# Performance work log

Hardware: AMD Instinct MI355X
Metric: run time of the kernel (lower is better)

The kernel has to match this reference:

```python
import jax, jax.numpy as jnp
from jax import lax
import numpy as np

N = 65536
D = 512
NUM_STEPS = 10
TIME_INTERVAL = 1.0


def setup_inputs() -> dict:
    key = jax.random.key(0)
    ks = jax.random.split(key, 8)
    s1 = 1.0 / np.sqrt(D + 1)
    s2 = 1.0 / np.sqrt(D)
    sg = 1.0 / np.sqrt(2 * D)
    return {
        "current_node_features": jax.random.normal(ks[0], (N, D), jnp.float32),
        "previous_hidden_state": jax.random.normal(ks[1], (N, D), jnp.float32),
        # torch nn.Linear layout: weight [out, in], bias [out]
        "W1": jax.random.uniform(ks[2], (D, D + 1), jnp.float32, -s1, s1),
        "b1": jax.random.uniform(ks[3], (D,), jnp.float32, -s1, s1),
        "W2": jax.random.uniform(ks[4], (D, D), jnp.float32, -s2, s2),
        "b2": jax.random.uniform(ks[5], (D,), jnp.float32, -s2, s2),
        "Wg": jax.random.uniform(ks[6], (D, 2 * D), jnp.float32, -sg, sg),
        "bg": jax.random.uniform(ks[7], (D,), jnp.float32, -sg, sg),
    }


def reference(current_node_features, previous_hidden_state, W1, b1, W2, b2, Wg, bg):
    x = current_node_features
    dt = jnp.asarray(TIME_INTERVAL / NUM_STEPS, x.dtype)
    n = x.shape[0]

    def euler_step(h, t):
        # concat time feature: [N, D+1]
        time_col = jnp.full((n, 1), t, h.dtype)
        z = jnp.concatenate([h, time_col], axis=-1)
        deriv = jnp.tanh(jnp.tanh(z @ W1.T + b1) @ W2.T + b2)
        return h + dt * deriv, None

    ts = jnp.arange(NUM_STEPS, dtype=x.dtype) * dt  # t_i = start + i*dt
    evolved, _ = lax.scan(euler_step, previous_hidden_state, ts)

    combined = jnp.concatenate([x, evolved], axis=-1)  # [N, 2D]
    gate = jax.nn.sigmoid(combined @ Wg.T + bg)
    updated = gate * evolved + (1.0 - gate) * x
    return updated, updated
```

## Files before the change

kernel.cpp:

```cpp
#include <hip/hip_runtime.h>

#define N_ROWS 65536
#define DIM    512
#define NSTEP  10

typedef float  f32x16 __attribute__((ext_vector_type(16)));
typedef float  f32x4  __attribute__((ext_vector_type(4)));
typedef short  s16x8  __attribute__((ext_vector_type(8)));
typedef __bf16 bf16x8 __attribute__((ext_vector_type(8)));
typedef unsigned int u32x2 __attribute__((ext_vector_type(2)));
typedef unsigned int u32x4 __attribute__((ext_vector_type(4)));

__device__ __forceinline__ unsigned f2bf(float f) {
  unsigned u = __float_as_uint(f);
  return (u + 0x7fffu + ((u >> 16) & 1u)) >> 16;
}
__device__ __forceinline__ unsigned pack2bf_rn(float a, float b) {
  unsigned ua = __float_as_uint(a) + 0x8000u;
  unsigned ub = __float_as_uint(b) + 0x8000u;
  return __builtin_amdgcn_perm(ub, ua, 0x07060302u);
}
#define LOG2E_X2 2.885390081777927f
#define LOG2E    1.442695040888963f
__device__ __forceinline__ float ftanh(float x) {
  float t = __builtin_amdgcn_exp2f(x * LOG2E_X2);
  float r = __builtin_amdgcn_rcpf(1.0f + t);
  return __builtin_fmaf(-2.0f, r, 1.0f);
}
__device__ __forceinline__ float fsigm(float x) {
  float t = __builtin_amdgcn_exp2f(-x * LOG2E);
  return __builtin_amdgcn_rcpf(1.0f + t);
}
__device__ __forceinline__ void mfma(f32x16& c, s16x8 a, s16x8 b) {
  c = __builtin_amdgcn_mfma_f32_32x32x16_bf16(
        __builtin_bit_cast(bf16x8, a), __builtin_bit_cast(bf16x8, b), c, 0, 0, 0);
}

__global__ void pack_frags_kernel(const float* __restrict__ src, int row_stride,
                                  int col_off, unsigned short* __restrict__ dst) {
  const int idx = blockIdx.x * 256 + threadIdx.x;
  const int l    = idx & 63;
  const int frag = idx >> 6;
  const int ks   = frag >> 4;
  const int otg  = frag & 15;
  const int o = otg * 32 + (l & 31);
  const int k = ks * 16 + (l >> 5) * 8;
  const float* p = src + (size_t)o * row_stride + col_off + k;
  s16x8 v;
#pragma unroll
  for (int i = 0; i < 8; ++i) v[i] = (short)f2bf(p[i]);
  *reinterpret_cast<s16x8*>(dst + (size_t)idx * 8) = v;
}

__global__ void c1_kernel(const float* __restrict__ W1, const float* __restrict__ b1,
                          float* __restrict__ c1) {
  const int o = threadIdx.x;
  const float wt = W1[(size_t)o * 513 + 512];
  const float bb = b1[o];
  for (int s = 0; s < NSTEP; ++s)
    c1[s * DIM + o] = bb + ((float)s * 0.1f) * wt;
}

__global__ __launch_bounds__(1024)
void ode_fused(const float* __restrict__ x, const float* __restrict__ h0,
               const float* __restrict__ b2, const float* __restrict__ bg,
               const unsigned short* __restrict__ w1f, const unsigned short* __restrict__ w2f,
               const unsigned short* __restrict__ wgaf, const unsigned short* __restrict__ wgbf,
               const float* __restrict__ c1, float* __restrict__ out)
{
  __shared__ char ldsT[64 * 1024];

  const int tid = threadIdx.x;
  const int w   = tid >> 6;
  const int l   = tid & 63;
  const int lm  = l & 31;
  const int h5  = l >> 5;
  const int m0  = blockIdx.x << 6;
  const int ow  = w << 5;
  const int rot = blockIdx.x & 31;

  {
    const int r  = tid >> 4;
    const int c0 = (tid & 15) << 2;
    const float* src = h0 + (size_t)(m0 + r) * DIM;
    char* trow = ldsT + r * 1024;
    const unsigned sw = (r & 7) << 4;
#pragma unroll
    for (int j = 0; j < 8; ++j) {
      const int c = c0 + (j << 6);
      f32x4 v = *reinterpret_cast<const f32x4*>(src + c);
      u32x2 pk;
      pk[0] = pack2bf_rn(v[0], v[1]);
      pk[1] = pack2bf_rn(v[2], v[3]);
      *reinterpret_cast<u32x2*>(trow + (((unsigned)(c << 1)) ^ sw)) = pk;
    }
  }

  f32x16 hst[2];
#pragma unroll
  for (int mt = 0; mt < 2; ++mt) {
    const float* hr = h0 + (size_t)(m0 + (mt << 5) + lm) * DIM;
#pragma unroll
    for (int g = 0; g < 4; ++g) {
      const int oc = ow + (g << 3) + (h5 << 2);
      f32x4 v = *reinterpret_cast<const f32x4*>(hr + oc);
#pragma unroll
      for (int j = 0; j < 4; ++j) hst[mt][(g << 2) + j] = v[j];
    }
  }

  const unsigned bm0 = (unsigned)lm << 10;
  const unsigned bm1 = (unsigned)(lm + 32) << 10;
  const unsigned sxm = (lm & 7) << 4;
  const unsigned kh  = (unsigned)h5 << 4;

  f32x16 acc[2];

  auto mm_lds = [&](const unsigned short* __restrict__ AF, const char* buf) {
    const s16x8* A = reinterpret_cast<const s16x8*>(AF);
#pragma unroll 4
    for (int ks = 0; ks < 32; ++ks) {
      const int kk = (ks + rot) & 31;
      s16x8 a = A[(((kk << 4) + w) << 6) + l];
      const unsigned ko = (((unsigned)kk << 5) + kh) ^ sxm;
      s16x8 b0 = *reinterpret_cast<const s16x8*>(buf + (bm0 + ko));
      s16x8 b1 = *reinterpret_cast<const s16x8*>(buf + (bm1 + ko));
      mfma(acc[0], a, b0);
      mfma(acc[1], a, b1);
    }
  };

  auto acc_init = [&](const float* __restrict__ vec) {
#pragma unroll
    for (int g = 0; g < 4; ++g) {
      const int oc = ow + (g << 3) + (h5 << 2);
      f32x4 v = *reinterpret_cast<const f32x4*>(vec + oc);
#pragma unroll
      for (int j = 0; j < 4; ++j) {
        acc[0][(g << 2) + j] = v[j];
        acc[1][(g << 2) + j] = v[j];
      }
    }
  };

  auto tile_write = [&](const f32x16 src[2], char* buf) {
#pragma unroll
    for (int mt = 0; mt < 2; ++mt) {
      const unsigned m = (unsigned)((mt << 5) + lm);
      char* trow = buf + (m << 10);
      const unsigned sw = (m & 7) << 4;
#pragma unroll
      for (int g = 0; g < 4; ++g) {
        const unsigned oc = (unsigned)(ow + (g << 3) + (h5 << 2));
        u32x2 pk;
        pk[0] = pack2bf_rn(src[mt][(g << 2) + 0], src[mt][(g << 2) + 1]);
        pk[1] = pack2bf_rn(src[mt][(g << 2) + 2], src[mt][(g << 2) + 3]);
        *reinterpret_cast<u32x2*>(trow + ((oc << 1) ^ sw)) = pk;
      }
    }
  };

  __syncthreads();

  for (int s = 0; s < NSTEP; ++s) {
    acc_init(c1 + s * DIM);
    mm_lds(w1f, ldsT);
#pragma unroll
    for (int mt = 0; mt < 2; ++mt)
#pragma unroll
      for (int i = 0; i < 16; ++i) acc[mt][i] = ftanh(acc[mt][i]);
    __syncthreads();
    tile_write(acc, ldsT);
    __syncthreads();
    acc_init(b2);
    mm_lds(w2f, ldsT);
#pragma unroll
    for (int mt = 0; mt < 2; ++mt)
#pragma unroll
      for (int i = 0; i < 16; ++i) {
        float t = __builtin_amdgcn_exp2f(acc[mt][i] * LOG2E_X2);
        float r = __builtin_amdgcn_rcpf(1.0f + t);
        hst[mt][i] = __builtin_fmaf(-0.2f, r, hst[mt][i] + 0.1f);
      }
    __syncthreads();
    tile_write(hst, ldsT);
    __syncthreads();
  }

  acc_init(bg);
  mm_lds(wgbf, ldsT);
  {
    const s16x8* A = reinterpret_cast<const s16x8*>(wgaf);
    const float* xr0 = x + (size_t)(m0 + lm) * DIM;
    const float* xr1 = x + (size_t)(m0 + 32 + lm) * DIM;
#pragma unroll 2
    for (int ks = 0; ks < 32; ++ks) {
      const int kk = (ks + rot) & 31;
      s16x8 a = A[(((kk << 4) + w) << 6) + l];
      const int kc = (kk << 4) + (h5 << 3);
      f32x4 u0 = *reinterpret_cast<const f32x4*>(xr0 + kc);
      f32x4 u1 = *reinterpret_cast<const f32x4*>(xr0 + kc + 4);
      u32x4 pb;
      pb[0] = pack2bf_rn(u0[0], u0[1]); pb[1] = pack2bf_rn(u0[2], u0[3]);
      pb[2] = pack2bf_rn(u1[0], u1[1]); pb[3] = pack2bf_rn(u1[2], u1[3]);
      s16x8 b0 = __builtin_bit_cast(s16x8, pb);
      f32x4 w0 = *reinterpret_cast<const f32x4*>(xr1 + kc);
      f32x4 w1 = *reinterpret_cast<const f32x4*>(xr1 + kc + 4);
      u32x4 qb;
      qb[0] = pack2bf_rn(w0[0], w0[1]); qb[1] = pack2bf_rn(w0[2], w0[3]);
      qb[2] = pack2bf_rn(w1[0], w1[1]); qb[3] = pack2bf_rn(w1[2], w1[3]);
      s16x8 b1 = __builtin_bit_cast(s16x8, qb);
      mfma(acc[0], a, b0);
      mfma(acc[1], a, b1);
    }
  }

  float* out1 = out + (size_t)N_ROWS * DIM;
#pragma unroll
  for (int mt = 0; mt < 2; ++mt) {
    const int m = m0 + (mt << 5) + lm;
    const float* xr = x + (size_t)m * DIM;
    float* o0p = out  + (size_t)m * DIM;
    float* o1p = out1 + (size_t)m * DIM;
#pragma unroll
    for (int g = 0; g < 4; ++g) {
      const int oc = ow + (g << 3) + (h5 << 2);
      f32x4 xv = *reinterpret_cast<const f32x4*>(xr + oc);
      f32x4 r;
#pragma unroll
      for (int j = 0; j < 4; ++j) {
        const float gt = fsigm(acc[mt][(g << 2) + j]);
        const float ev = hst[mt][(g << 2) + j];
        r[j] = gt * ev + (1.0f - gt) * xv[j];
      }
      *reinterpret_cast<f32x4*>(o0p + oc) = r;
      *reinterpret_cast<f32x4*>(o1p + oc) = r;
    }
  }
}

extern "C" void kernel_launch(void* const* d_in, const int* in_sizes, int n_in,
                              void* d_out, int out_size, void* d_ws, size_t ws_size,
                              hipStream_t stream) {
  const float* x  = (const float*)d_in[0];
  const float* h0 = (const float*)d_in[1];
  const float* W1 = (const float*)d_in[2];
  const float* b1 = (const float*)d_in[3];
  const float* W2 = (const float*)d_in[4];
  const float* b2 = (const float*)d_in[5];
  const float* Wg = (const float*)d_in[6];
  const float* bg = (const float*)d_in[7];

  char* ws = (char*)d_ws;
  const size_t FRAG_BYTES = (size_t)512 * 512 * 2;
  unsigned short* w1f  = (unsigned short*)(ws + 0 * FRAG_BYTES);
  unsigned short* w2f  = (unsigned short*)(ws + 1 * FRAG_BYTES);
  unsigned short* wgaf = (unsigned short*)(ws + 2 * FRAG_BYTES);
  unsigned short* wgbf = (unsigned short*)(ws + 3 * FRAG_BYTES);
  float*          c1   = (float*)(ws + 4 * FRAG_BYTES);

  pack_frags_kernel<<<128, 256, 0, stream>>>(W1, 513, 0,   w1f);
  pack_frags_kernel<<<128, 256, 0, stream>>>(W2, 512, 0,   w2f);
  pack_frags_kernel<<<128, 256, 0, stream>>>(Wg, 1024, 0,  wgaf);
  pack_frags_kernel<<<128, 256, 0, stream>>>(Wg, 1024, 512, wgbf);
  c1_kernel<<<1, 512, 0, stream>>>(W1, b1, c1);

  ode_fused<<<N_ROWS / 64, 1024, 0, stream>>>(x, h0, b2, bg, w1f, w2f, wgaf, wgbf,
                                              c1, (float*)d_out);
}
```

Measured before the change: 1.048 ms.

## Store activations and weights in MFMA fragment order for linear loads

Repacks the weight fragments so each wave's output-tile group is contiguous across k-steps. The LDS activation tile is also stored directly in MFMA B-fragment order, so every lane reads a contiguous 16-byte slot. This drops the XOR swizzle, the per-block k-rotation and the address arithmetic in the inner GEMM loop, and the loops are fully unrolled. It risks LDS bank conflicts on the 8-byte tile writes, and without the rotation all blocks hit the same weight addresses at once.

```diff
diff --git a/kernel.cpp b/kernel.cpp
--- a/kernel.cpp
+++ b/kernel.cpp
@@ -41,8 +41,8 @@
   const int idx = blockIdx.x * 256 + threadIdx.x;
   const int l    = idx & 63;
   const int frag = idx >> 6;
-  const int ks   = frag >> 4;
-  const int otg  = frag & 15;
+  const int otg  = frag >> 5;
+  const int ks   = frag & 31;
   const int o = otg * 32 + (l & 31);
   const int k = ks * 16 + (l >> 5) * 8;
   const float* p = src + (size_t)o * row_stride + col_off + k;
@@ -64,8 +64,8 @@
 __global__ __launch_bounds__(1024)
 void ode_fused(const float* __restrict__ x, const float* __restrict__ h0,
                const float* __restrict__ b2, const float* __restrict__ bg,
-               const unsigned short* __restrict__ w1f, const unsigned short* __restrict__ w2f,
-               const unsigned short* __restrict__ wgaf, const unsigned short* __restrict__ wgbf,
+               const s16x8* __restrict__ w1f, const s16x8* __restrict__ w2f,
+               const s16x8* __restrict__ wgaf, const s16x8* __restrict__ wgbf,
                const float* __restrict__ c1, float* __restrict__ out)
 {
   __shared__ char ldsT[64 * 1024];
@@ -77,22 +77,22 @@
   const int h5  = l >> 5;
   const int m0  = blockIdx.x << 6;
   const int ow  = w << 5;
-  const int rot = blockIdx.x & 31;
+  const unsigned lbyte = (unsigned)l << 4;
 
   {
-    const int r  = tid >> 4;
-    const int c0 = (tid & 15) << 2;
-    const float* src = h0 + (size_t)(m0 + r) * DIM;
-    char* trow = ldsT + r * 1024;
-    const unsigned sw = (r & 7) << 4;
-#pragma unroll
-    for (int j = 0; j < 8; ++j) {
-      const int c = c0 + (j << 6);
-      f32x4 v = *reinterpret_cast<const f32x4*>(src + c);
-      u32x2 pk;
-      pk[0] = pack2bf_rn(v[0], v[1]);
-      pk[1] = pack2bf_rn(v[2], v[3]);
-      *reinterpret_cast<u32x2*>(trow + (((unsigned)(c << 1)) ^ sw)) = pk;
+#pragma unroll
+    for (int q = 0; q < 2; ++q) {
+      const int ks = (w << 1) | q;
+#pragma unroll
+      for (int mt = 0; mt < 2; ++mt) {
+        const float* src = h0 + (size_t)(m0 + (mt << 5) + lm) * DIM + (ks << 4) + (h5 << 3);
+        f32x4 v0 = *reinterpret_cast<const f32x4*>(src);
+        f32x4 v1 = *reinterpret_cast<const f32x4*>(src + 4);
+        u32x4 pk;
+        pk[0] = pack2bf_rn(v0[0], v0[1]); pk[1] = pack2bf_rn(v0[2], v0[3]);
+        pk[2] = pack2bf_rn(v1[0], v1[1]); pk[3] = pack2bf_rn(v1[2], v1[3]);
+        *reinterpret_cast<u32x4*>(ldsT + (((ks << 1) | mt) << 10) + lbyte) = pk;
+      }
     }
   }
 
@@ -109,22 +109,15 @@
     }
   }
 
-  const unsigned bm0 = (unsigned)lm << 10;
-  const unsigned bm1 = (unsigned)(lm + 32) << 10;
-  const unsigned sxm = (lm & 7) << 4;
-  const unsigned kh  = (unsigned)h5 << 4;
-
   f32x16 acc[2];
 
-  auto mm_lds = [&](const unsigned short* __restrict__ AF, const char* buf) {
-    const s16x8* A = reinterpret_cast<const s16x8*>(AF);
-#pragma unroll 4
+  auto mm_lds = [&](const s16x8* __restrict__ A) {
+    const s16x8* Aw = A + (w << 11);
+#pragma unroll
     for (int ks = 0; ks < 32; ++ks) {
-      const int kk = (ks + rot) & 31;
-      s16x8 a = A[(((kk << 4) + w) << 6) + l];
-      const unsigned ko = (((unsigned)kk << 5) + kh) ^ sxm;
-      s16x8 b0 = *reinterpret_cast<const s16x8*>(buf + (bm0 + ko));
-      s16x8 b1 = *reinterpret_cast<const s16x8*>(buf + (bm1 + ko));
+      s16x8 a  = Aw[(ks << 6) + l];
+      s16x8 b0 = *reinterpret_cast<const s16x8*>(ldsT + (ks << 11) + lbyte);
+      s16x8 b1 = *reinterpret_cast<const s16x8*>(ldsT + (ks << 11) + 1024 + lbyte);
       mfma(acc[0], a, b0);
       mfma(acc[1], a, b1);
     }
@@ -143,37 +136,33 @@
     }
   };
 
-  auto tile_write = [&](const f32x16 src[2], char* buf) {
-#pragma unroll
-    for (int mt = 0; mt < 2; ++mt) {
-      const unsigned m = (unsigned)((mt << 5) + lm);
-      char* trow = buf + (m << 10);
-      const unsigned sw = (m & 7) << 4;
+  auto tile_write = [&](const f32x16 src[2]) {
+    const unsigned base = ((unsigned)w << 12) + ((unsigned)lm << 4) + ((unsigned)h5 << 3);
+#pragma unroll
+    for (int mt = 0; mt < 2; ++mt)
 #pragma unroll
       for (int g = 0; g < 4; ++g) {
-        const unsigned oc = (unsigned)(ow + (g << 3) + (h5 << 2));
         u32x2 pk;
         pk[0] = pack2bf_rn(src[mt][(g << 2) + 0], src[mt][(g << 2) + 1]);
         pk[1] = pack2bf_rn(src[mt][(g << 2) + 2], src[mt][(g << 2) + 3]);
-        *reinterpret_cast<u32x2*>(trow + ((oc << 1) ^ sw)) = pk;
-      }
-    }
+        *reinterpret_cast<u32x2*>(ldsT + base + ((g >> 1) << 11) + (mt << 10) + ((g & 1) << 9)) = pk;
+      }
   };
 
   __syncthreads();
 
   for (int s = 0; s < NSTEP; ++s) {
     acc_init(c1 + s * DIM);
-    mm_lds(w1f, ldsT);
+    mm_lds(w1f);
 #pragma unroll
     for (int mt = 0; mt < 2; ++mt)
 #pragma unroll
       for (int i = 0; i < 16; ++i) acc[mt][i] = ftanh(acc[mt][i]);
     __syncthreads();
-    tile_write(acc, ldsT);
+    tile_write(acc);
     __syncthreads();
     acc_init(b2);
-    mm_lds(w2f, ldsT);
+    mm_lds(w2f);
 #pragma unroll
     for (int mt = 0; mt < 2; ++mt)
 #pragma unroll
@@ -183,21 +172,20 @@
         hst[mt][i] = __builtin_fmaf(-0.2f, r, hst[mt][i] + 0.1f);
       }
     __syncthreads();
-    tile_write(hst, ldsT);
+    tile_write(hst);
     __syncthreads();
   }
 
   acc_init(bg);
-  mm_lds(wgbf, ldsT);
+  mm_lds(wgbf);
   {
-    const s16x8* A = reinterpret_cast<const s16x8*>(wgaf);
-    const float* xr0 = x + (size_t)(m0 + lm) * DIM;
-    const float* xr1 = x + (size_t)(m0 + 32 + lm) * DIM;
-#pragma unroll 2
+    const s16x8* Aw = wgaf + (w << 11);
+    const float* xr0 = x + (size_t)(m0 + lm) * DIM + (h5 << 3);
+    const float* xr1 = xr0 + (size_t)32 * DIM;
+#pragma unroll 4
     for (int ks = 0; ks < 32; ++ks) {
-      const int kk = (ks + rot) & 31;
-      s16x8 a = A[(((kk << 4) + w) << 6) + l];
-      const int kc = (kk << 4) + (h5 << 3);
+      s16x8 a = Aw[(ks << 6) + l];
+      const int kc = ks << 4;
       f32x4 u0 = *reinterpret_cast<const f32x4*>(xr0 + kc);
       f32x4 u1 = *reinterpret_cast<const f32x4*>(xr0 + kc + 4);
       u32x4 pb;
@@ -265,6 +253,8 @@
   pack_frags_kernel<<<128, 256, 0, stream>>>(Wg, 1024, 512, wgbf);
   c1_kernel<<<1, 512, 0, stream>>>(W1, b1, c1);
 
-  ode_fused<<<N_ROWS / 64, 1024, 0, stream>>>(x, h0, b2, bg, w1f, w2f, wgaf, wgbf,
+  ode_fused<<<N_ROWS / 64, 1024, 0, stream>>>(x, h0, b2, bg,
+                                              (const s16x8*)w1f, (const s16x8*)w2f,
+                                              (const s16x8*)wgaf, (const s16x8*)wgbf,
                                               c1, (float*)d_out);
 }
```

Result: slower. 2.064 ms (+96.9%).
